# Kernel tuning notes

Hardware: AMD Instinct MI355X
Metric: run time of the kernel (lower is better)

Reference implementation:

```python
import jax, jax.numpy as jnp
import numpy as np

B, N, F_IN, F_OUT = 8, 2048, 512, 512


def setup_inputs() -> dict:
    key = jax.random.key(0)
    k1, k2, k3, k4 = jax.random.split(key, 4)
    X = jax.random.normal(k1, (B, N, F_IN), dtype=jnp.float32)
    A = jax.random.uniform(k2, (B, N, N), dtype=jnp.float32)
    # nn.Linear params (kaiming-uniform-ish scale is irrelevant for correctness)
    bound = 1.0 / np.sqrt(F_IN)
    W = jax.random.uniform(k3, (F_IN, F_OUT), dtype=jnp.float32, minval=-bound, maxval=bound)
    b = jax.random.uniform(k4, (F_OUT,), dtype=jnp.float32, minval=-bound, maxval=bound)
    return {"X": X, "A": A, "W": W, "b": b}


def reference(X, A, W, b):
    # A' = A + I  (self-loops)
    A_hat = A + jnp.eye(A.shape[-1], dtype=A.dtype)
    # D^{-1/2}: per-row degree of A'.  torch builds diag_embed + two bmms;
    # mathematically identical to broadcasted row/column scaling.
    d_inv_sqrt = A_hat.sum(axis=-1) ** -0.5                      # [B, N]
    L = A_hat * d_inv_sqrt[:, :, None] * d_inv_sqrt[:, None, :]  # [B, N, N]
    x = X @ W + b                                                # [B, N, F_out]
    return jnp.einsum('bij,bjf->bif', L, x)
```

## Files before the change

kernel.cpp:

```cpp
#include <hip/hip_runtime.h>

#define B_ 8
#define N_ 2048
#define FIN_ 512
#define FOUT_ 512

typedef __attribute__((ext_vector_type(8))) short short8;
typedef __attribute__((ext_vector_type(4))) float floatx4;
typedef __attribute__((ext_vector_type(4))) unsigned short ushortx4;
typedef __attribute__((ext_vector_type(8))) unsigned short ushortx8;

__device__ inline unsigned short f2bf(float f) {
    union { float f; unsigned int u; } x; x.f = f;
    unsigned int r = x.u + 0x7FFFu + ((x.u >> 16) & 1u);
    return (unsigned short)(r >> 16);
}

__device__ inline void glds16(const void* g, void* l) {
    __builtin_amdgcn_global_load_lds(
        (const __attribute__((address_space(1))) void*)g,
        (__attribute__((address_space(3))) void*)l, 16, 0, 0);
}

__global__ __launch_bounds__(256) void degree_cast_kernel(
    const float* __restrict__ A, float* __restrict__ dinv,
    unsigned short* __restrict__ Abf) {
    int row = blockIdx.x;
    size_t base = (size_t)row * N_;
    const float4* A4 = (const float4*)(A + base);
    int t = threadIdx.x;
    float4 v0 = A4[t];
    float4 v1 = A4[t + 256];
    ushortx4 p0, p1;
    p0[0] = f2bf(v0.x); p0[1] = f2bf(v0.y); p0[2] = f2bf(v0.z); p0[3] = f2bf(v0.w);
    p1[0] = f2bf(v1.x); p1[1] = f2bf(v1.y); p1[2] = f2bf(v1.z); p1[3] = f2bf(v1.w);
    *(ushortx4*)(Abf + base + t * 4) = p0;
    *(ushortx4*)(Abf + base + (t + 256) * 4) = p1;
    float s = v0.x + v0.y + v0.z + v0.w + v1.x + v1.y + v1.z + v1.w;
#pragma unroll
    for (int off = 32; off > 0; off >>= 1) s += __shfl_down(s, off, 64);
    __shared__ float red[4];
    if ((t & 63) == 0) red[t >> 6] = s;
    __syncthreads();
    if (t == 0) dinv[row] = rsqrtf(red[0] + red[1] + red[2] + red[3] + 1.0f);
}

__global__ __launch_bounds__(256) void castX_kernel(const float* __restrict__ X,
                                                    unsigned short* __restrict__ Xbf) {
    size_t e0 = ((size_t)blockIdx.x * 256 + threadIdx.x) * 8;
    float4 a0 = *(const float4*)(X + e0);
    float4 a1 = *(const float4*)(X + e0 + 4);
    float av[8] = {a0.x, a0.y, a0.z, a0.w, a1.x, a1.y, a1.z, a1.w};
    ushortx8 p;
#pragma unroll
    for (int r = 0; r < 8; ++r) p[r] = f2bf(av[r]);
    *(ushortx8*)(Xbf + e0) = p;
}

__global__ __launch_bounds__(256) void transposeW_kernel(const float* __restrict__ W,
                                                         unsigned short* __restrict__ Wt) {
    __shared__ float tile[32][33];
    int bx = blockIdx.x * 32;
    int by = blockIdx.y * 32;
    int tx = threadIdx.x, ty = threadIdx.y;
#pragma unroll
    for (int r = 0; r < 32; r += 8)
        tile[ty + r][tx] = W[(size_t)(by + ty + r) * FOUT_ + bx + tx];
    __syncthreads();
#pragma unroll
    for (int r = 0; r < 32; r += 8)
        Wt[(size_t)(bx + ty + r) * FIN_ + by + tx] = f2bf(tile[tx][ty + r]);
}


__global__ __launch_bounds__(256) void gemm1_kernel(
    const unsigned short* __restrict__ Abase,
    const unsigned short* __restrict__ Btbase,
    unsigned short* __restrict__ XwT,
    const float* __restrict__ bias,
    const float* __restrict__ dinv) {
    __shared__ __align__(16) char smem[65536];

    int t = threadIdx.x;
    int lane = t & 63;
    int wave = t >> 6;
    int wr = wave >> 1, wc = wave & 1;
    int q = lane >> 4, m = lane & 15;
    int n0 = blockIdx.x * 128;
    int m0 = blockIdx.y * 128;

    int srow = t >> 3;
    int scol = (((t & 7) ^ (srow & 7)) * 8);
    int x0 = ((q ^ (m & 7)) * 16);
    int x1 = x0 ^ 64;

    floatx4 acc[4][4];
#pragma unroll
    for (int mi = 0; mi < 4; ++mi)
#pragma unroll
        for (int ni = 0; ni < 4; ++ni)
            acc[mi][ni] = (floatx4){0.f, 0.f, 0.f, 0.f};

    const unsigned short* gA = Abase + (size_t)(m0 + srow) * FIN_ + scol;
    const unsigned short* gB = Btbase + (size_t)(n0 + srow) * FIN_ + scol;

#define STAGE1(bufi) do {                                              \
        char* lA = smem + (bufi) * 32768 + wave * 1024;                \
        char* lB = smem + (bufi) * 32768 + 16384 + wave * 1024;        \
        _Pragma("unroll")                                              \
        for (int u = 0; u < 4; ++u) {                                  \
            glds16(gA + (size_t)(u * 32) * FIN_, lA + u * 4096);       \
            glds16(gB + (size_t)(u * 32) * FIN_, lB + u * 4096);       \
        }                                                              \
        gA += 64; gB += 64;                                            \
    } while (0)

    STAGE1(0);
    STAGE1(1);

    const int NT = FIN_ / 64;
    for (int kt = 0; kt < NT; ++kt) {
        if (kt < NT - 1) asm volatile("s_waitcnt vmcnt(8)" ::: "memory");
        else             asm volatile("s_waitcnt vmcnt(0)" ::: "memory");
        __builtin_amdgcn_sched_barrier(0);
        __builtin_amdgcn_s_barrier();
        const char* As = smem + (kt & 1) * 32768;
        const char* Bs = As + 16384;
        short8 af0[4], bf0[4], af1[4], bf1[4];
#pragma unroll
        for (int mi = 0; mi < 4; ++mi)
            af0[mi] = *(const short8*)(As + (wr * 64 + mi * 16 + m) * 128 + x0);
#pragma unroll
        for (int ni = 0; ni < 4; ++ni)
            bf0[ni] = *(const short8*)(Bs + (wc * 64 + ni * 16 + m) * 128 + x0);
#pragma unroll
        for (int mi = 0; mi < 4; ++mi)
            af1[mi] = *(const short8*)(As + (wr * 64 + mi * 16 + m) * 128 + x1);
#pragma unroll
        for (int ni = 0; ni < 4; ++ni)
            bf1[ni] = *(const short8*)(Bs + (wc * 64 + ni * 16 + m) * 128 + x1);
        asm volatile("s_waitcnt lgkmcnt(8)" ::: "memory");
        __builtin_amdgcn_sched_barrier(0);
        __builtin_amdgcn_s_setprio(1);
#pragma unroll
        for (int mi = 0; mi < 4; ++mi)
#pragma unroll
            for (int ni = 0; ni < 4; ++ni)
                acc[mi][ni] = __builtin_amdgcn_mfma_f32_16x16x32_bf16(
                    af0[mi], bf0[ni], acc[mi][ni], 0, 0, 0);
        __builtin_amdgcn_s_setprio(0);
        asm volatile("s_waitcnt lgkmcnt(0)" ::: "memory");
        __builtin_amdgcn_sched_barrier(0);
        __builtin_amdgcn_s_barrier();
        if (kt + 2 < NT) STAGE1(kt & 1);
        __builtin_amdgcn_sched_barrier(0);
        __builtin_amdgcn_s_setprio(1);
#pragma unroll
        for (int mi = 0; mi < 4; ++mi)
#pragma unroll
            for (int ni = 0; ni < 4; ++ni)
                acc[mi][ni] = __builtin_amdgcn_mfma_f32_16x16x32_bf16(
                    af1[mi], bf1[ni], acc[mi][ni], 0, 0, 0);
        __builtin_amdgcn_s_setprio(0);
    }
#undef STAGE1

    unsigned short* T = (unsigned short*)smem;
#pragma unroll
    for (int mi = 0; mi < 4; ++mi) {
        int row = wr * 64 + mi * 16 + q * 4;
        float4 dv = *(const float4*)(dinv + m0 + row);
        float dr[4] = {dv.x, dv.y, dv.z, dv.w};
#pragma unroll
        for (int ni = 0; ni < 4; ++ni) {
            int col = wc * 64 + ni * 16 + m;
            float bv = bias[n0 + col];
            ushortx4 pk;
#pragma unroll
            for (int r = 0; r < 4; ++r) pk[r] = f2bf((acc[mi][ni][r] + bv) * dr[r]);
            *(ushortx4*)(T + col * 136 + row) = pk;
        }
    }
    __syncthreads();
    int f  = t >> 1;
    int c0 = (t & 1) * 64;
    int bb = m0 >> 11;
    int node0 = (m0 & 2047) + c0;
    unsigned short* dst = XwT + ((size_t)bb * FOUT_ + n0 + f) * N_ + node0;
    const unsigned short* src = T + f * 136 + c0;
#pragma unroll
    for (int u = 0; u < 8; ++u)
        *(ushortx8*)(dst + u * 8) = *(const ushortx8*)(src + u * 8);
}

__global__ __launch_bounds__(256) void gemm2_kernel(
    const unsigned short* __restrict__ Abf,
    const unsigned short* __restrict__ XwT,
    const float* __restrict__ dinv,
    float* __restrict__ out) {
    __shared__ __align__(16) char smem[65536];

    int t = threadIdx.x;
    int lane = t & 63;
    int wave = t >> 6;
    int wr = wave >> 1, wc = wave & 1;
    int q = lane >> 4, m = lane & 15;

    int id = blockIdx.x;
    int b  = id & 7;
    int s  = id >> 3;
    int n0 = (s & 3) * 128;
    int m0 = (s >> 2) * 128;

    const unsigned short* Ab = Abf + (size_t)b * N_ * N_;
    const unsigned short* Bb = XwT + (size_t)b * FOUT_ * N_;

    int srow = t >> 3;
    int scol = (((t & 7) ^ (srow & 7)) * 8);
    int x0 = ((q ^ (m & 7)) * 16);
    int x1 = x0 ^ 64;

    floatx4 acc[4][4];
#pragma unroll
    for (int mi = 0; mi < 4; ++mi)
#pragma unroll
        for (int ni = 0; ni < 4; ++ni)
            acc[mi][ni] = (floatx4){0.f, 0.f, 0.f, 0.f};

    const unsigned short* gA = Ab + (size_t)(m0 + srow) * N_ + scol;
    const unsigned short* gB = Bb + (size_t)(n0 + srow) * N_ + scol;

#define STAGE2(bufi) do {                                              \
        char* lA = smem + (bufi) * 32768 + wave * 1024;                \
        char* lB = smem + (bufi) * 32768 + 16384 + wave * 1024;        \
        _Pragma("unroll")                                              \
        for (int u = 0; u < 4; ++u) {                                  \
            glds16(gA + (size_t)(u * 32) * N_, lA + u * 4096);         \
            glds16(gB + (size_t)(u * 32) * N_, lB + u * 4096);         \
        }                                                              \
        gA += 64; gB += 64;                                            \
    } while (0)

    STAGE2(0);
    STAGE2(1);

    const int NT = N_ / 64;
    for (int kt = 0; kt < NT; ++kt) {
        if (kt < NT - 1) asm volatile("s_waitcnt vmcnt(8)" ::: "memory");
        else             asm volatile("s_waitcnt vmcnt(0)" ::: "memory");
        __builtin_amdgcn_sched_barrier(0);
        __builtin_amdgcn_s_barrier();
        const char* As = smem + (kt & 1) * 32768;
        const char* Bs = As + 16384;
        short8 af0[4], bf0[4], af1[4], bf1[4];
#pragma unroll
        for (int mi = 0; mi < 4; ++mi)
            af0[mi] = *(const short8*)(As + (wr * 64 + mi * 16 + m) * 128 + x0);
#pragma unroll
        for (int ni = 0; ni < 4; ++ni)
            bf0[ni] = *(const short8*)(Bs + (wc * 64 + ni * 16 + m) * 128 + x0);
#pragma unroll
        for (int mi = 0; mi < 4; ++mi)
            af1[mi] = *(const short8*)(As + (wr * 64 + mi * 16 + m) * 128 + x1);
#pragma unroll
        for (int ni = 0; ni < 4; ++ni)
            bf1[ni] = *(const short8*)(Bs + (wc * 64 + ni * 16 + m) * 128 + x1);
        asm volatile("s_waitcnt lgkmcnt(8)" ::: "memory");
        __builtin_amdgcn_sched_barrier(0);
        __builtin_amdgcn_s_setprio(1);
#pragma unroll
        for (int mi = 0; mi < 4; ++mi)
#pragma unroll
            for (int ni = 0; ni < 4; ++ni)
                acc[mi][ni] = __builtin_amdgcn_mfma_f32_16x16x32_bf16(
                    af0[mi], bf0[ni], acc[mi][ni], 0, 0, 0);
        __builtin_amdgcn_s_setprio(0);
        asm volatile("s_waitcnt lgkmcnt(0)" ::: "memory");
        __builtin_amdgcn_sched_barrier(0);
        __builtin_amdgcn_s_barrier();
        if (kt + 2 < NT) STAGE2(kt & 1);
        __builtin_amdgcn_sched_barrier(0);
        __builtin_amdgcn_s_setprio(1);
#pragma unroll
        for (int mi = 0; mi < 4; ++mi)
#pragma unroll
            for (int ni = 0; ni < 4; ++ni)
                acc[mi][ni] = __builtin_amdgcn_mfma_f32_16x16x32_bf16(
                    af1[mi], bf1[ni], acc[mi][ni], 0, 0, 0);
        __builtin_amdgcn_s_setprio(0);
    }
#undef STAGE2

    float* C = out + (size_t)b * N_ * FOUT_;
#pragma unroll
    for (int mi = 0; mi < 4; ++mi) {
        int rowb = m0 + wr * 64 + mi * 16 + q * 4;
        float4 dv = *(const float4*)(dinv + b * N_ + rowb);
        float dr[4] = {dv.x, dv.y, dv.z, dv.w};
#pragma unroll
        for (int ni = 0; ni < 4; ++ni) {
            int col = n0 + wc * 64 + ni * 16 + m;
            ushortx4 yv = *(const ushortx4*)(Bb + (size_t)col * N_ + rowb);
#pragma unroll
            for (int r = 0; r < 4; ++r) {
                union { unsigned int u; float f; } yc; yc.u = ((unsigned int)yv[r]) << 16;
                C[(size_t)(rowb + r) * FOUT_ + col] = dr[r] * (acc[mi][ni][r] + yc.f);
            }
        }
    }
}

extern "C" void kernel_launch(void* const* d_in, const int* in_sizes, int n_in,
                              void* d_out, int out_size, void* d_ws, size_t ws_size,
                              hipStream_t stream) {
    const float* X    = (const float*)d_in[0];
    const float* A    = (const float*)d_in[1];
    const float* W    = (const float*)d_in[2];
    const float* bias = (const float*)d_in[3];
    float* out = (float*)d_out;
    char* ws = (char*)d_ws;

    float* dinv          = (float*)(ws);
    unsigned short* Xbf  = (unsigned short*)(ws + (1u << 16));
    unsigned short* Wt   = (unsigned short*)(ws + (1u << 16) + 16777216u);
    unsigned short* XwT  = (unsigned short*)(ws + (1u << 16) + 16777216u + 524288u);
    unsigned short* Abf  = (unsigned short*)(ws + (1u << 16) + 16777216u + 524288u + 16777216u);

    degree_cast_kernel<<<B_ * N_, 256, 0, stream>>>(A, dinv, Abf);
    castX_kernel<<<((size_t)B_ * N_ * FIN_) / 2048, 256, 0, stream>>>(X, Xbf);
    transposeW_kernel<<<dim3(FOUT_ / 32, FIN_ / 32), dim3(32, 8), 0, stream>>>(W, Wt);

    gemm1_kernel<<<dim3(FOUT_ / 128, (B_ * N_) / 128), 256, 0, stream>>>(
        Xbf, Wt, XwT, bias, dinv);

    gemm2_kernel<<<512, 256, 0, stream>>>(Abf, XwT, dinv, out);
}
```

Measured before the change: 284.6 us.

## Retile aggregation GEMM to 64x512 blocks with 8 waves, drop double buffering

Each block now covers 64 rows of A against all 512 output features, using 512 threads where each wave owns a 64-column slice. A is read from global memory once per row block instead of once per column tile, which cuts A traffic. The grid halves to 256 blocks. The double-buffered, barrier-scheduled pipeline is replaced by a single-buffered loop with two __syncthreads per k-step, so load latency is no longer overlapped with MFMA work. The large B tile in LDS also limits occupancy to one block per CU.

```diff
diff --git a/kernel.cpp b/kernel.cpp
--- a/kernel.cpp
+++ b/kernel.cpp
@@ -193,24 +193,23 @@
         *(ushortx8*)(dst + u * 8) = *(const ushortx8*)(src + u * 8);
 }
 
-__global__ __launch_bounds__(256) void gemm2_kernel(
+__global__ __launch_bounds__(512) void gemm2_kernel(
     const unsigned short* __restrict__ Abf,
     const unsigned short* __restrict__ XwT,
     const float* __restrict__ dinv,
     float* __restrict__ out) {
-    __shared__ __align__(16) char smem[65536];
+    __shared__ __align__(16) char smem[73728];
+    char* As = smem;
+    char* Bs = smem + 8192;
 
     int t = threadIdx.x;
     int lane = t & 63;
     int wave = t >> 6;
-    int wr = wave >> 1, wc = wave & 1;
     int q = lane >> 4, m = lane & 15;
 
     int id = blockIdx.x;
-    int b  = id & 7;
-    int s  = id >> 3;
-    int n0 = (s & 3) * 128;
-    int m0 = (s >> 2) * 128;
+    int b    = id & 7;
+    int m0   = (id >> 3) * 64;
 
     const unsigned short* Ab = Abf + (size_t)b * N_ * N_;
     const unsigned short* Bb = XwT + (size_t)b * FOUT_ * N_;
@@ -228,78 +227,47 @@
             acc[mi][ni] = (floatx4){0.f, 0.f, 0.f, 0.f};
 
     const unsigned short* gA = Ab + (size_t)(m0 + srow) * N_ + scol;
-    const unsigned short* gB = Bb + (size_t)(n0 + srow) * N_ + scol;
-
-#define STAGE2(bufi) do {                                              \
-        char* lA = smem + (bufi) * 32768 + wave * 1024;                \
-        char* lB = smem + (bufi) * 32768 + 16384 + wave * 1024;        \
-        _Pragma("unroll")                                              \
-        for (int u = 0; u < 4; ++u) {                                  \
-            glds16(gA + (size_t)(u * 32) * N_, lA + u * 4096);         \
-            glds16(gB + (size_t)(u * 32) * N_, lB + u * 4096);         \
-        }                                                              \
-        gA += 64; gB += 64;                                            \
-    } while (0)
-
-    STAGE2(0);
-    STAGE2(1);
-
-    const int NT = N_ / 64;
-    for (int kt = 0; kt < NT; ++kt) {
-        if (kt < NT - 1) asm volatile("s_waitcnt vmcnt(8)" ::: "memory");
-        else             asm volatile("s_waitcnt vmcnt(0)" ::: "memory");
-        __builtin_amdgcn_sched_barrier(0);
-        __builtin_amdgcn_s_barrier();
-        const char* As = smem + (kt & 1) * 32768;
-        const char* Bs = As + 16384;
-        short8 af0[4], bf0[4], af1[4], bf1[4];
-#pragma unroll
-        for (int mi = 0; mi < 4; ++mi)
-            af0[mi] = *(const short8*)(As + (wr * 64 + mi * 16 + m) * 128 + x0);
-#pragma unroll
-        for (int ni = 0; ni < 4; ++ni)
-            bf0[ni] = *(const short8*)(Bs + (wc * 64 + ni * 16 + m) * 128 + x0);
-#pragma unroll
-        for (int mi = 0; mi < 4; ++mi)
-            af1[mi] = *(const short8*)(As + (wr * 64 + mi * 16 + m) * 128 + x1);
-#pragma unroll
-        for (int ni = 0; ni < 4; ++ni)
-            bf1[ni] = *(const short8*)(Bs + (wc * 64 + ni * 16 + m) * 128 + x1);
-        asm volatile("s_waitcnt lgkmcnt(8)" ::: "memory");
-        __builtin_amdgcn_sched_barrier(0);
-        __builtin_amdgcn_s_setprio(1);
-#pragma unroll
-        for (int mi = 0; mi < 4; ++mi)
+    const unsigned short* gB = Bb + (size_t)srow * N_ + scol;
+    char* lA = As + wave * 1024;
+    char* lB = Bs + wave * 1024;
+
+    for (int kt = 0; kt < N_ / 64; ++kt) {
+        glds16(gA, lA);
+#pragma unroll
+        for (int u = 0; u < 8; ++u)
+            glds16(gB + (size_t)(u * 64) * N_, lB + u * 8192);
+        gA += 64; gB += 64;
+        __syncthreads();
+
+#pragma unroll
+        for (int sl = 0; sl < 2; ++sl) {
+            int xs = sl ? x1 : x0;
+            short8 af[4], bfr[4];
+#pragma unroll
+            for (int mi = 0; mi < 4; ++mi)
+                af[mi] = *(const short8*)(As + (mi * 16 + m) * 128 + xs);
 #pragma unroll
             for (int ni = 0; ni < 4; ++ni)
-                acc[mi][ni] = __builtin_amdgcn_mfma_f32_16x16x32_bf16(
-                    af0[mi], bf0[ni], acc[mi][ni], 0, 0, 0);
-        __builtin_amdgcn_s_setprio(0);
-        asm volatile("s_waitcnt lgkmcnt(0)" ::: "memory");
-        __builtin_amdgcn_sched_barrier(0);
-        __builtin_amdgcn_s_barrier();
-        if (kt + 2 < NT) STAGE2(kt & 1);
-        __builtin_amdgcn_sched_barrier(0);
-        __builtin_amdgcn_s_setprio(1);
-#pragma unroll
-        for (int mi = 0; mi < 4; ++mi)
-#pragma unroll
-            for (int ni = 0; ni < 4; ++ni)
-                acc[mi][ni] = __builtin_amdgcn_mfma_f32_16x16x32_bf16(
-                    af1[mi], bf1[ni], acc[mi][ni], 0, 0, 0);
-        __builtin_amdgcn_s_setprio(0);
+                bfr[ni] = *(const short8*)(Bs + (wave * 64 + ni * 16 + m) * 128 + xs);
+#pragma unroll
+            for (int mi = 0; mi < 4; ++mi)
+#pragma unroll
+                for (int ni = 0; ni < 4; ++ni)
+                    acc[mi][ni] = __builtin_amdgcn_mfma_f32_16x16x32_bf16(
+                        af[mi], bfr[ni], acc[mi][ni], 0, 0, 0);
+        }
+        __syncthreads();
     }
-#undef STAGE2
 
     float* C = out + (size_t)b * N_ * FOUT_;
 #pragma unroll
     for (int mi = 0; mi < 4; ++mi) {
-        int rowb = m0 + wr * 64 + mi * 16 + q * 4;
+        int rowb = m0 + mi * 16 + q * 4;
         float4 dv = *(const float4*)(dinv + b * N_ + rowb);
         float dr[4] = {dv.x, dv.y, dv.z, dv.w};
 #pragma unroll
         for (int ni = 0; ni < 4; ++ni) {
-            int col = n0 + wc * 64 + ni * 16 + m;
+            int col = wave * 64 + ni * 16 + m;
             ushortx4 yv = *(const ushortx4*)(Bb + (size_t)col * N_ + rowb);
 #pragma unroll
             for (int r = 0; r < 4; ++r) {
@@ -333,5 +301,5 @@
     gemm1_kernel<<<dim3(FOUT_ / 128, (B_ * N_) / 128), 256, 0, stream>>>(
         Xbf, Wt, XwT, bias, dinv);
 
-    gemm2_kernel<<<512, 256, 0, stream>>>(Abf, XwT, dinv, out);
-}
+    gemm2_kernel<<<256, 512, 0, stream>>>(Abf, XwT, dinv, out);
+}
```

New measurement: 318.8 us. 12.0% more time.
